# Optimization experiments

Measured on AMD Instinct MI355X. Metric: run time of the kernel, lower is better.

The kernel has to match this reference:

```python
import jax, jax.numpy as jnp
import numpy as np

T, B, I, H = 2048, 64, 512, 512
SIGMA = 0.01


def setup_inputs() -> dict:
    key = jax.random.key(0)
    ks = jax.random.split(key, 9)
    d = {
        "X": jax.random.normal(ks[0], (T, B, I), dtype=jnp.float32),
        "W_xf": jax.random.normal(ks[1], (I, H), dtype=jnp.float32) * SIGMA,
        "W_hf": jax.random.normal(ks[2], (H, H), dtype=jnp.float32) * SIGMA,
        "b_f": jnp.ones((H,), dtype=jnp.float32),
        "W_xi": jax.random.normal(ks[3], (I, H), dtype=jnp.float32) * SIGMA,
        "W_hi": jax.random.normal(ks[4], (H, H), dtype=jnp.float32) * SIGMA,
        "b_i": jnp.zeros((H,), dtype=jnp.float32),
        "W_xo": jax.random.normal(ks[5], (I, H), dtype=jnp.float32) * SIGMA,
        "W_ho": jax.random.normal(ks[6], (H, H), dtype=jnp.float32) * SIGMA,
        "b_o": jnp.zeros((H,), dtype=jnp.float32),
        "W_xc": jax.random.normal(ks[7], (I, H), dtype=jnp.float32) * SIGMA,
        "W_hc": jax.random.normal(ks[8], (H, H), dtype=jnp.float32) * SIGMA,
        "b_c": jnp.zeros((H,), dtype=jnp.float32),
    }
    return d


def reference(X, W_xf, W_hf, b_f, W_xi, W_hi, b_i, W_xo, W_ho, b_o, W_xc, W_hc, b_c):
    batch = X.shape[1]
    hidden = W_hf.shape[0]
    # Fuse the 4 input-side GEMMs into one [T*B, I] @ [I, 4H] GEMM (same math,
    # just batched over time since X is not part of the recurrence).
    W_x = jnp.concatenate([W_xf, W_xi, W_xo, W_xc], axis=1)           # [I, 4H]
    W_h = jnp.concatenate([W_hf, W_hi, W_ho, W_hc], axis=1)           # [H, 4H]
    b = jnp.concatenate([b_f, b_i, b_o, b_c], axis=0)                 # [4H]
    Xg = jnp.einsum('tbi,ih->tbh', X, W_x) + b                        # [T, B, 4H]

    h0 = jnp.zeros((batch, hidden), dtype=X.dtype)
    c0 = jnp.zeros((batch, hidden), dtype=X.dtype)

    def step(carry, xg):
        h, c = carry
        g = xg + h @ W_h                                              # [B, 4H]
        f = jax.nn.sigmoid(g[:, 0 * hidden:1 * hidden])
        i = jax.nn.sigmoid(g[:, 1 * hidden:2 * hidden])
        o = jax.nn.sigmoid(g[:, 2 * hidden:3 * hidden])
        c_hat = jnp.tanh(g[:, 3 * hidden:4 * hidden])
        c_new = f * c + i * c_hat
        h_new = o * jnp.tanh(c_new)
        return (h_new, c_new), h_new

    (h_T, c_T), outputs = jax.lax.scan(step, (h0, c0), Xg)
    return outputs, h_T, c_T
```

## Files before the change

### kernel.cpp

```cpp
#include <hip/hip_runtime.h>
#include <stdint.h>


typedef __attribute__((ext_vector_type(8))) short short8;
typedef __attribute__((ext_vector_type(4))) float f32x4;

#define T_STEPS 2048
#define GB 4
#define GH 64
#define FSTRIDE 16

__device__ __forceinline__ unsigned short f2bf(float f) {
  unsigned int x = __float_as_uint(f);
  x += 0x7fffu + ((x >> 16) & 1u);
  return (unsigned short)(x >> 16);
}
__device__ __forceinline__ float bf2f(unsigned short u) {
  return __uint_as_float(((unsigned int)u) << 16);
}
__device__ __forceinline__ void gl2lds16(const void* g, void* lds) {
  __builtin_amdgcn_global_load_lds(
      (const __attribute__((address_space(1))) void*)(uintptr_t)g,
      (__attribute__((address_space(3))) void*)(unsigned int)(uintptr_t)lds,
      16, 0, 0);
}


__global__ __launch_bounds__(256) void cast_x_kernel(
    const float* __restrict__ X, unsigned short* __restrict__ Xb) {
  long long i = ((long long)blockIdx.x * 256 + threadIdx.x) * 8;
  float4 a = *(const float4*)(X + i);
  float4 b = *(const float4*)(X + i + 4);
  union { short8 v; unsigned short u[8]; } o;
  o.u[0] = f2bf(a.x); o.u[1] = f2bf(a.y); o.u[2] = f2bf(a.z); o.u[3] = f2bf(a.w);
  o.u[4] = f2bf(b.x); o.u[5] = f2bf(b.y); o.u[6] = f2bf(b.z); o.u[7] = f2bf(b.w);
  *(short8*)(Xb + i) = o.v;
}

__global__ __launch_bounds__(256) void pack_w_kernel(
    const float* __restrict__ Wf, const float* __restrict__ Wi,
    const float* __restrict__ Wo, const float* __restrict__ Wc,
    unsigned short* __restrict__ Wt) {
  int n = blockIdx.x;
  int g = n >> 9, h = n & 511;
  const float* W = (g == 0) ? Wf : (g == 1) ? Wi : (g == 2) ? Wo : Wc;
  for (int k = threadIdx.x; k < 512; k += 256)
    Wt[(size_t)n * 512 + k] = f2bf(W[(size_t)k * 512 + h]);
}

__global__ __launch_bounds__(256) void init_kernel(unsigned short* hbuf, int* flags) {
  int i = blockIdx.x * 256 + threadIdx.x;
  if (i < 2 * 64 * 512) hbuf[i] = 0;
  if (i < GB * GH * FSTRIDE) flags[i] = 0;
}

__global__ __launch_bounds__(256) void gemm_xg_kernel(
    const unsigned short* __restrict__ A, const unsigned short* __restrict__ Bt,
    unsigned short* __restrict__ C) {
  __shared__ unsigned short As[128 * 64];
  __shared__ unsigned short Bs[128 * 64];
  const int tid = threadIdx.x;
  const int lane = tid & 63, wave = tid >> 6;
  const int bm = blockIdx.x, bn = blockIdx.y;
  const int wm = (wave & 1) * 64, wn = (wave >> 1) * 64;

  f32x4 acc[4][4];
#pragma unroll
  for (int i = 0; i < 4; ++i)
#pragma unroll
    for (int j = 0; j < 4; ++j) acc[i][j] = (f32x4){0.f, 0.f, 0.f, 0.f};

  for (int kt = 0; kt < 512; kt += 64) {
    __syncthreads();
#pragma unroll
    for (int r = 0; r < 4; ++r) {
      int chunk = r * 256 + tid;
      int row = chunk >> 3, c8 = chunk & 7;
      gl2lds16(A + ((size_t)(bm * 128 + row) * 512 + kt + c8 * 8),
               (void*)(As + (size_t)(r * 256 + wave * 64) * 8));
      gl2lds16(Bt + ((size_t)(bn * 128 + row) * 512 + kt + c8 * 8),
               (void*)(Bs + (size_t)(r * 256 + wave * 64) * 8));
    }
    __syncthreads();
#pragma unroll
    for (int kc = 0; kc < 64; kc += 32) {
      const int ko = kc + (lane >> 4) * 8;
      short8 av[4], bv[4];
#pragma unroll
      for (int mt = 0; mt < 4; ++mt)
        av[mt] = *(const short8*)(As + (wm + mt * 16 + (lane & 15)) * 64 + ko);
#pragma unroll
      for (int nt = 0; nt < 4; ++nt)
        bv[nt] = *(const short8*)(Bs + (wn + nt * 16 + (lane & 15)) * 64 + ko);
#pragma unroll
      for (int mt = 0; mt < 4; ++mt)
#pragma unroll
        for (int nt = 0; nt < 4; ++nt)
          acc[mt][nt] = __builtin_amdgcn_mfma_f32_16x16x32_bf16(
              av[mt], bv[nt], acc[mt][nt], 0, 0, 0);
    }
  }
  const int q = lane >> 4, cidx = lane & 15;
#pragma unroll
  for (int mt = 0; mt < 4; ++mt)
#pragma unroll
    for (int nt = 0; nt < 4; ++nt)
#pragma unroll
      for (int r = 0; r < 4; ++r) {
        int row = wm + mt * 16 + q * 4 + r;
        int col = wn + nt * 16 + cidx;
        C[(size_t)(bm * 128 + row) * 2048 + bn * 128 + col] = f2bf(acc[mt][nt][r]);
      }
}

__global__ __launch_bounds__(256) void lstm_rec_kernel(
    const unsigned short* __restrict__ Xg,
    const unsigned short* __restrict__ Wht,
    const float* __restrict__ b_f, const float* __restrict__ b_i,
    const float* __restrict__ b_o, const float* __restrict__ b_c,
    float* __restrict__ out, unsigned short* hbuf, int* flags) {
  const int tid = threadIdx.x;
  const int lane = tid & 63, wave = tid >> 6;
  const int gb = blockIdx.x >> 6;
  const int gh = blockIdx.x & 63;

  __shared__ unsigned short Wl[32][520];
  __shared__ float Cred[4][16][33];

  for (int idx = tid; idx < 32 * 64; idx += 256) {
    int cc = idx >> 6, k8 = idx & 63;
    int n = (cc >> 3) * 512 + gh * 8 + (cc & 7);
    short8 v = *(const short8*)(Wht + (size_t)n * 512 + k8 * 8);
    *(short8*)(&Wl[cc][k8 * 8]) = v;
  }

  float creg = 0.f;
  float bias0 = 0.f, bias1 = 0.f, bias2 = 0.f, bias3 = 0.f;
  int bb = 0, jj = 0;
  if (tid < 128) {
    bb = tid >> 3; jj = tid & 7;
    int col = gh * 8 + jj;
    bias0 = b_f[col]; bias1 = b_i[col]; bias2 = b_o[col]; bias3 = b_c[col];
  }
  __syncthreads();

  const int myflag = (gb * GH + gh) * FSTRIDE;

  for (int t = 0; t < T_STEPS; ++t) {
    float xg0 = 0.f, xg1 = 0.f, xg2 = 0.f, xg3 = 0.f;
    if (tid < 128) {
      const unsigned short* xr =
          Xg + ((size_t)t * 64 + gb * 16 + bb) * 2048 + gh * 8 + jj;
      xg0 = bf2f(xr[0]); xg1 = bf2f(xr[512]); xg2 = bf2f(xr[1024]); xg3 = bf2f(xr[1536]);
    }
    if (t > 0) {
      if (tid < GH) {
        const int* fp = flags + (gb * GH + tid) * FSTRIDE;
        while (__hip_atomic_load(fp, __ATOMIC_RELAXED, __HIP_MEMORY_SCOPE_AGENT) < t)
          __builtin_amdgcn_s_sleep(1);
      }
      __syncthreads();
      __builtin_amdgcn_fence(__ATOMIC_ACQUIRE, "workgroup");
    }
    const unsigned short* hrow =
        hbuf + ((size_t)(t & 1) * 64 * 512) + (size_t)gb * 16 * 512;
    f32x4 acc0 = {0.f, 0.f, 0.f, 0.f}, acc1 = {0.f, 0.f, 0.f, 0.f};
    const int m = lane & 15, quad = lane >> 4;
#pragma unroll
    for (int kc = 0; kc < 128; kc += 32) {
      int k = wave * 128 + kc + quad * 8;
      const unsigned long long* ap =
          (const unsigned long long*)(hrow + (size_t)m * 512 + k);
      union { short8 v; unsigned long long q[2]; } au;
      au.q[0] = __hip_atomic_load(ap, __ATOMIC_RELAXED, __HIP_MEMORY_SCOPE_AGENT);
      au.q[1] = __hip_atomic_load(ap + 1, __ATOMIC_RELAXED, __HIP_MEMORY_SCOPE_AGENT);
      short8 bfr0 = *(const short8*)(&Wl[m][k]);
      short8 bfr1 = *(const short8*)(&Wl[16 + m][k]);
      acc0 = __builtin_amdgcn_mfma_f32_16x16x32_bf16(au.v, bfr0, acc0, 0, 0, 0);
      acc1 = __builtin_amdgcn_mfma_f32_16x16x32_bf16(au.v, bfr1, acc1, 0, 0, 0);
    }
#pragma unroll
    for (int r = 0; r < 4; ++r) {
      Cred[wave][quad * 4 + r][m] = acc0[r];
      Cred[wave][quad * 4 + r][16 + m] = acc1[r];
    }
    __syncthreads();
    if (tid < 128) {
      float gf = Cred[0][bb][jj] + Cred[1][bb][jj] + Cred[2][bb][jj] + Cred[3][bb][jj];
      float gi = Cred[0][bb][8+jj] + Cred[1][bb][8+jj] + Cred[2][bb][8+jj] + Cred[3][bb][8+jj];
      float go = Cred[0][bb][16+jj] + Cred[1][bb][16+jj] + Cred[2][bb][16+jj] + Cred[3][bb][16+jj];
      float gc = Cred[0][bb][24+jj] + Cred[1][bb][24+jj] + Cred[2][bb][24+jj] + Cred[3][bb][24+jj];
      gf += bias0 + xg0; gi += bias1 + xg1; go += bias2 + xg2; gc += bias3 + xg3;
      float f  = 1.f / (1.f + __expf(-gf));
      float ii = 1.f / (1.f + __expf(-gi));
      float oo = 1.f / (1.f + __expf(-go));
      float ch = 1.f - 2.f / (1.f + __expf(2.f * gc));
      creg = f * creg + ii * ch;
      float tc = 1.f - 2.f / (1.f + __expf(2.f * creg));
      float h = oo * tc;
      size_t orow = ((size_t)t * 64 + gb * 16 + bb) * 512 + gh * 8 + jj;
      out[orow] = h;
      __hip_atomic_store(hbuf + ((size_t)((t + 1) & 1) * 64 * 512) +
                             (size_t)(gb * 16 + bb) * 512 + gh * 8 + jj,
                         f2bf(h), __ATOMIC_RELAXED, __HIP_MEMORY_SCOPE_AGENT);
      if (t == T_STEPS - 1) {
        size_t base = (size_t)T_STEPS * 64 * 512;
        out[base + (size_t)(gb * 16 + bb) * 512 + gh * 8 + jj] = h;
        out[base + 64 * 512 + (size_t)(gb * 16 + bb) * 512 + gh * 8 + jj] = creg;
      }
    }
    __syncthreads();
    __builtin_amdgcn_fence(__ATOMIC_RELEASE, "workgroup");
    if (tid == 0)
      __hip_atomic_store(flags + myflag, t + 1, __ATOMIC_RELAXED,
                         __HIP_MEMORY_SCOPE_AGENT);
  }
}


extern "C" void kernel_launch(void* const* d_in, const int* in_sizes, int n_in,
                              void* d_out, int out_size, void* d_ws, size_t ws_size,
                              hipStream_t stream) {
  const float* X    = (const float*)d_in[0];
  const float* W_xf = (const float*)d_in[1];
  const float* W_hf = (const float*)d_in[2];
  const float* b_f  = (const float*)d_in[3];
  const float* W_xi = (const float*)d_in[4];
  const float* W_hi = (const float*)d_in[5];
  const float* b_i  = (const float*)d_in[6];
  const float* W_xo = (const float*)d_in[7];
  const float* W_ho = (const float*)d_in[8];
  const float* b_o  = (const float*)d_in[9];
  const float* W_xc = (const float*)d_in[10];
  const float* W_hc = (const float*)d_in[11];
  const float* b_c  = (const float*)d_in[12];
  float* out = (float*)d_out;

  char* ws = (char*)d_ws;
  unsigned short* Xb   = (unsigned short*)(ws + 0LL);
  unsigned short* Xg   = (unsigned short*)(ws + 134217728LL);
  unsigned short* Wxt  = (unsigned short*)(ws + 671088640LL);
  unsigned short* Wht  = (unsigned short*)(ws + 673185792LL);
  unsigned short* hbuf = (unsigned short*)(ws + 675282944LL);
  int* flags           = (int*)(ws + 675414016LL);

  cast_x_kernel<<<dim3(32768), dim3(256), 0, stream>>>(X, Xb);
  pack_w_kernel<<<dim3(2048), dim3(256), 0, stream>>>(W_xf, W_xi, W_xo, W_xc, Wxt);
  pack_w_kernel<<<dim3(2048), dim3(256), 0, stream>>>(W_hf, W_hi, W_ho, W_hc, Wht);
  init_kernel<<<dim3(256), dim3(256), 0, stream>>>(hbuf, flags);
  gemm_xg_kernel<<<dim3(1024, 16), dim3(256), 0, stream>>>(Xb, Wxt, Xg);
  lstm_rec_kernel<<<dim3(256), dim3(256), 0, stream>>>(Xg, Wht, b_f, b_i, b_o, b_c,
                                                       out, hbuf, flags);
}
```

Baseline: 5.993 ms.

## Replace per-block flag barrier with step-tagged hidden-state words

Drops the per-block flag array and its spin-wait barrier. Each hidden value is now stored as a 32-bit word holding the bf16 value and the low 16 bits of the step index. Consumers spin directly on the words they read until every tag matches the current step, which removes the flag poll, a block barrier and the release/acquire fences from the critical path. In exchange each h read is twice as wide and split into eight 32-bit atomic loads with a retry loop. hbuf is moved to reuse the start of the workspace (the Xb region) and is initialised after the GEMM.

```diff
diff --git a/kernel.cpp b/kernel.cpp
--- a/kernel.cpp
+++ b/kernel.cpp
@@ -6,9 +6,7 @@
 typedef __attribute__((ext_vector_type(4))) float f32x4;
 
 #define T_STEPS 2048
-#define GB 4
-#define GH 64
-#define FSTRIDE 16
+#define SLOT (64 * 512)
 
 __device__ __forceinline__ unsigned short f2bf(float f) {
   unsigned int x = __float_as_uint(f);
@@ -48,10 +46,9 @@
     Wt[(size_t)n * 512 + k] = f2bf(W[(size_t)k * 512 + h]);
 }
 
-__global__ __launch_bounds__(256) void init_kernel(unsigned short* hbuf, int* flags) {
+__global__ __launch_bounds__(256) void init_kernel(unsigned int* hbuf) {
   int i = blockIdx.x * 256 + threadIdx.x;
-  if (i < 2 * 64 * 512) hbuf[i] = 0;
-  if (i < GB * GH * FSTRIDE) flags[i] = 0;
+  if (i < 2 * SLOT) hbuf[i] = 0u;
 }
 
 __global__ __launch_bounds__(256) void gemm_xg_kernel(
@@ -118,7 +115,7 @@
     const unsigned short* __restrict__ Wht,
     const float* __restrict__ b_f, const float* __restrict__ b_i,
     const float* __restrict__ b_o, const float* __restrict__ b_c,
-    float* __restrict__ out, unsigned short* hbuf, int* flags) {
+    float* __restrict__ out, unsigned int* hbuf) {
   const int tid = threadIdx.x;
   const int lane = tid & 63, wave = tid >> 6;
   const int gb = blockIdx.x >> 6;
@@ -144,7 +141,7 @@
   }
   __syncthreads();
 
-  const int myflag = (gb * GH + gh) * FSTRIDE;
+  const int m = lane & 15, quad = lane >> 4;
 
   for (int t = 0; t < T_STEPS; ++t) {
     float xg0 = 0.f, xg1 = 0.f, xg2 = 0.f, xg3 = 0.f;
@@ -153,27 +150,32 @@
           Xg + ((size_t)t * 64 + gb * 16 + bb) * 2048 + gh * 8 + jj;
       xg0 = bf2f(xr[0]); xg1 = bf2f(xr[512]); xg2 = bf2f(xr[1024]); xg3 = bf2f(xr[1536]);
     }
-    if (t > 0) {
-      if (tid < GH) {
-        const int* fp = flags + (gb * GH + tid) * FSTRIDE;
-        while (__hip_atomic_load(fp, __ATOMIC_RELAXED, __HIP_MEMORY_SCOPE_AGENT) < t)
-          __builtin_amdgcn_s_sleep(1);
-      }
-      __syncthreads();
-      __builtin_amdgcn_fence(__ATOMIC_ACQUIRE, "workgroup");
-    }
-    const unsigned short* hrow =
-        hbuf + ((size_t)(t & 1) * 64 * 512) + (size_t)gb * 16 * 512;
+    const unsigned int tg = (unsigned int)t & 0xffffu;
+    const unsigned int* hcur =
+        hbuf + (size_t)(t & 1) * SLOT + (size_t)(gb * 16 + m) * 512;
     f32x4 acc0 = {0.f, 0.f, 0.f, 0.f}, acc1 = {0.f, 0.f, 0.f, 0.f};
-    const int m = lane & 15, quad = lane >> 4;
 #pragma unroll
     for (int kc = 0; kc < 128; kc += 32) {
-      int k = wave * 128 + kc + quad * 8;
-      const unsigned long long* ap =
-          (const unsigned long long*)(hrow + (size_t)m * 512 + k);
-      union { short8 v; unsigned long long q[2]; } au;
-      au.q[0] = __hip_atomic_load(ap, __ATOMIC_RELAXED, __HIP_MEMORY_SCOPE_AGENT);
-      au.q[1] = __hip_atomic_load(ap + 1, __ATOMIC_RELAXED, __HIP_MEMORY_SCOPE_AGENT);
+      const int k = wave * 128 + kc + quad * 8;
+      const unsigned int* ap = hcur + k;
+      unsigned int w0, w1, w2, w3, w4, w5, w6, w7, bad;
+      do {
+        w0 = __hip_atomic_load(ap + 0, __ATOMIC_RELAXED, __HIP_MEMORY_SCOPE_AGENT);
+        w1 = __hip_atomic_load(ap + 1, __ATOMIC_RELAXED, __HIP_MEMORY_SCOPE_AGENT);
+        w2 = __hip_atomic_load(ap + 2, __ATOMIC_RELAXED, __HIP_MEMORY_SCOPE_AGENT);
+        w3 = __hip_atomic_load(ap + 3, __ATOMIC_RELAXED, __HIP_MEMORY_SCOPE_AGENT);
+        w4 = __hip_atomic_load(ap + 4, __ATOMIC_RELAXED, __HIP_MEMORY_SCOPE_AGENT);
+        w5 = __hip_atomic_load(ap + 5, __ATOMIC_RELAXED, __HIP_MEMORY_SCOPE_AGENT);
+        w6 = __hip_atomic_load(ap + 6, __ATOMIC_RELAXED, __HIP_MEMORY_SCOPE_AGENT);
+        w7 = __hip_atomic_load(ap + 7, __ATOMIC_RELAXED, __HIP_MEMORY_SCOPE_AGENT);
+        bad = ((w0 ^ tg) | (w1 ^ tg) | (w2 ^ tg) | (w3 ^ tg) |
+               (w4 ^ tg) | (w5 ^ tg) | (w6 ^ tg) | (w7 ^ tg)) & 0xffffu;
+      } while (bad != 0u);
+      union { short8 v; unsigned int u[4]; } au;
+      au.u[0] = (w0 >> 16) | (w1 & 0xffff0000u);
+      au.u[1] = (w2 >> 16) | (w3 & 0xffff0000u);
+      au.u[2] = (w4 >> 16) | (w5 & 0xffff0000u);
+      au.u[3] = (w6 >> 16) | (w7 & 0xffff0000u);
       short8 bfr0 = *(const short8*)(&Wl[m][k]);
       short8 bfr1 = *(const short8*)(&Wl[16 + m][k]);
       acc0 = __builtin_amdgcn_mfma_f32_16x16x32_bf16(au.v, bfr0, acc0, 0, 0, 0);
@@ -200,9 +202,11 @@
       float h = oo * tc;
       size_t orow = ((size_t)t * 64 + gb * 16 + bb) * 512 + gh * 8 + jj;
       out[orow] = h;
-      __hip_atomic_store(hbuf + ((size_t)((t + 1) & 1) * 64 * 512) +
+      unsigned int word =
+          ((unsigned int)f2bf(h) << 16) | ((unsigned int)(t + 1) & 0xffffu);
+      __hip_atomic_store(hbuf + (size_t)((t + 1) & 1) * SLOT +
                              (size_t)(gb * 16 + bb) * 512 + gh * 8 + jj,
-                         f2bf(h), __ATOMIC_RELAXED, __HIP_MEMORY_SCOPE_AGENT);
+                         word, __ATOMIC_RELAXED, __HIP_MEMORY_SCOPE_AGENT);
       if (t == T_STEPS - 1) {
         size_t base = (size_t)T_STEPS * 64 * 512;
         out[base + (size_t)(gb * 16 + bb) * 512 + gh * 8 + jj] = h;
@@ -210,10 +214,6 @@
       }
     }
     __syncthreads();
-    __builtin_amdgcn_fence(__ATOMIC_RELEASE, "workgroup");
-    if (tid == 0)
-      __hip_atomic_store(flags + myflag, t + 1, __ATOMIC_RELAXED,
-                         __HIP_MEMORY_SCOPE_AGENT);
   }
 }
 
@@ -241,14 +241,13 @@
   unsigned short* Xg   = (unsigned short*)(ws + 134217728LL);
   unsigned short* Wxt  = (unsigned short*)(ws + 671088640LL);
   unsigned short* Wht  = (unsigned short*)(ws + 673185792LL);
-  unsigned short* hbuf = (unsigned short*)(ws + 675282944LL);
-  int* flags           = (int*)(ws + 675414016LL);
+  unsigned int* hbuf   = (unsigned int*)(ws + 0LL);
 
   cast_x_kernel<<<dim3(32768), dim3(256), 0, stream>>>(X, Xb);
   pack_w_kernel<<<dim3(2048), dim3(256), 0, stream>>>(W_xf, W_xi, W_xo, W_xc, Wxt);
   pack_w_kernel<<<dim3(2048), dim3(256), 0, stream>>>(W_hf, W_hi, W_ho, W_hc, Wht);
-  init_kernel<<<dim3(256), dim3(256), 0, stream>>>(hbuf, flags);
   gemm_xg_kernel<<<dim3(1024, 16), dim3(256), 0, stream>>>(Xb, Wxt, Xg);
+  init_kernel<<<dim3(256), dim3(256), 0, stream>>>(hbuf);
   lstm_rec_kernel<<<dim3(256), dim3(256), 0, stream>>>(Xg, Wht, b_f, b_i, b_o, b_c,
-                                                       out, hbuf, flags);
-}
+                                                       out, hbuf);
+}
```

New measurement: 12.66 ms. 2.11x slower.

## Repartition LSTM recurrence to 64 blocks with register-resident recurrent weights

Applied to the files above, without the earlier changes.

The recurrent kernel moves from 256 blocks (8 hidden columns each) to 64 blocks (32 hidden columns each). Each wave owns one gate and holds its slice of W_h in registers, which removes the LDS weight reads and the cross-wave K reduction. Fewer blocks means fewer flags to poll per step, and the spin loop no longer sleeps. The h loads now use cache-bypassing inline asm, and hbuf and flags are placed in the workspace region of Xb, which is dead once the GEMM has run. The cost is heavy register pressure and more MFMA work per block on the serial step path.

```diff
diff --git a/kernel.cpp b/kernel.cpp
--- a/kernel.cpp
+++ b/kernel.cpp
@@ -4,11 +4,9 @@
 
 typedef __attribute__((ext_vector_type(8))) short short8;
 typedef __attribute__((ext_vector_type(4))) float f32x4;
+typedef __attribute__((ext_vector_type(4))) unsigned int u32x4;
 
 #define T_STEPS 2048
-#define GB 4
-#define GH 64
-#define FSTRIDE 16
 
 __device__ __forceinline__ unsigned short f2bf(float f) {
   unsigned int x = __float_as_uint(f);
@@ -48,10 +46,10 @@
     Wt[(size_t)n * 512 + k] = f2bf(W[(size_t)k * 512 + h]);
 }
 
-__global__ __launch_bounds__(256) void init_kernel(unsigned short* hbuf, int* flags) {
+__global__ __launch_bounds__(256) void init_kernel(unsigned int* hbuf, int* flags) {
   int i = blockIdx.x * 256 + threadIdx.x;
-  if (i < 2 * 64 * 512) hbuf[i] = 0;
-  if (i < GB * GH * FSTRIDE) flags[i] = 0;
+  if (i < 2 * 64 * 256) hbuf[i] = 0u;
+  if (i < 64) flags[i] = 0;
 }
 
 __global__ __launch_bounds__(256) void gemm_xg_kernel(
@@ -113,107 +111,119 @@
       }
 }
 
-__global__ __launch_bounds__(256) void lstm_rec_kernel(
+__global__ __launch_bounds__(256, 1) void lstm_rec_kernel(
     const unsigned short* __restrict__ Xg,
     const unsigned short* __restrict__ Wht,
     const float* __restrict__ b_f, const float* __restrict__ b_i,
     const float* __restrict__ b_o, const float* __restrict__ b_c,
-    float* __restrict__ out, unsigned short* hbuf, int* flags) {
+    float* __restrict__ out, unsigned int* hbuf, int* flags) {
   const int tid = threadIdx.x;
   const int lane = tid & 63, wave = tid >> 6;
-  const int gb = blockIdx.x >> 6;
-  const int gh = blockIdx.x & 63;
-
-  __shared__ unsigned short Wl[32][520];
-  __shared__ float Cred[4][16][33];
-
-  for (int idx = tid; idx < 32 * 64; idx += 256) {
-    int cc = idx >> 6, k8 = idx & 63;
-    int n = (cc >> 3) * 512 + gh * 8 + (cc & 7);
-    short8 v = *(const short8*)(Wht + (size_t)n * 512 + k8 * 8);
-    *(short8*)(&Wl[cc][k8 * 8]) = v;
+  const int gb = blockIdx.x >> 4;
+  const int gh = blockIdx.x & 15;
+  const int m = lane & 15, quad = lane >> 4;
+
+  __shared__ float Glds[4][16][34];
+
+  short8 bw0[16], bw1[16];
+  {
+    const unsigned short* wb = Wht + ((size_t)wave * 512 + gh * 32) * 512;
+#pragma unroll
+    for (int s = 0; s < 16; ++s) {
+      bw0[s] = *(const short8*)(wb + (size_t)m * 512 + s * 32 + quad * 8);
+      bw1[s] = *(const short8*)(wb + (size_t)(16 + m) * 512 + s * 32 + quad * 8);
+    }
   }
 
-  float creg = 0.f;
-  float bias0 = 0.f, bias1 = 0.f, bias2 = 0.f, bias3 = 0.f;
-  int bb = 0, jj = 0;
-  if (tid < 128) {
-    bb = tid >> 3; jj = tid & 7;
-    int col = gh * 8 + jj;
-    bias0 = b_f[col]; bias1 = b_i[col]; bias2 = b_o[col]; bias3 = b_c[col];
-  }
-  __syncthreads();
-
-  const int myflag = (gb * GH + gh) * FSTRIDE;
+  const int b = tid >> 4, p = tid & 15;
+  const int j0 = gh * 32 + 2 * p;
+  const float2 bf_f = *(const float2*)(b_f + j0);
+  const float2 bf_i = *(const float2*)(b_i + j0);
+  const float2 bf_o = *(const float2*)(b_o + j0);
+  const float2 bf_c = *(const float2*)(b_c + j0);
+  float c0 = 0.f, c1 = 0.f;
+
+  const int myflag = gb * 16 + gh;
 
   for (int t = 0; t < T_STEPS; ++t) {
-    float xg0 = 0.f, xg1 = 0.f, xg2 = 0.f, xg3 = 0.f;
-    if (tid < 128) {
-      const unsigned short* xr =
-          Xg + ((size_t)t * 64 + gb * 16 + bb) * 2048 + gh * 8 + jj;
-      xg0 = bf2f(xr[0]); xg1 = bf2f(xr[512]); xg2 = bf2f(xr[1024]); xg3 = bf2f(xr[1536]);
+    unsigned int xgw0, xgw1, xgw2, xgw3;
+    {
+      const unsigned int* xr =
+          (const unsigned int*)(Xg + ((size_t)t * 64 + gb * 16 + b) * 2048) +
+          gh * 16 + p;
+      xgw0 = xr[0]; xgw1 = xr[256]; xgw2 = xr[512]; xgw3 = xr[768];
     }
     if (t > 0) {
-      if (tid < GH) {
-        const int* fp = flags + (gb * GH + tid) * FSTRIDE;
-        while (__hip_atomic_load(fp, __ATOMIC_RELAXED, __HIP_MEMORY_SCOPE_AGENT) < t)
-          __builtin_amdgcn_s_sleep(1);
+      if (tid < 16) {
+        const int* fp = flags + gb * 16 + tid;
+        while (__hip_atomic_load(fp, __ATOMIC_RELAXED,
+                                 __HIP_MEMORY_SCOPE_AGENT) < t) {}
       }
       __syncthreads();
       __builtin_amdgcn_fence(__ATOMIC_ACQUIRE, "workgroup");
     }
-    const unsigned short* hrow =
-        hbuf + ((size_t)(t & 1) * 64 * 512) + (size_t)gb * 16 * 512;
+    const char* hq = (const char*)hbuf + (size_t)(t & 1) * 65536 +
+                     (size_t)(gb * 16 + m) * 1024 + (size_t)quad * 16;
+    u32x4 hv[16];
+#pragma unroll
+    for (int s = 0; s < 16; ++s)
+      asm volatile("global_load_dwordx4 %0, %1, off sc0 sc1"
+                   : "=&v"(hv[s]) : "v"(hq + s * 64) : "memory");
+    asm volatile("s_waitcnt vmcnt(0)" ::: "memory");
+    __builtin_amdgcn_sched_barrier(0);
+
     f32x4 acc0 = {0.f, 0.f, 0.f, 0.f}, acc1 = {0.f, 0.f, 0.f, 0.f};
-    const int m = lane & 15, quad = lane >> 4;
-#pragma unroll
-    for (int kc = 0; kc < 128; kc += 32) {
-      int k = wave * 128 + kc + quad * 8;
-      const unsigned long long* ap =
-          (const unsigned long long*)(hrow + (size_t)m * 512 + k);
-      union { short8 v; unsigned long long q[2]; } au;
-      au.q[0] = __hip_atomic_load(ap, __ATOMIC_RELAXED, __HIP_MEMORY_SCOPE_AGENT);
-      au.q[1] = __hip_atomic_load(ap + 1, __ATOMIC_RELAXED, __HIP_MEMORY_SCOPE_AGENT);
-      short8 bfr0 = *(const short8*)(&Wl[m][k]);
-      short8 bfr1 = *(const short8*)(&Wl[16 + m][k]);
-      acc0 = __builtin_amdgcn_mfma_f32_16x16x32_bf16(au.v, bfr0, acc0, 0, 0, 0);
-      acc1 = __builtin_amdgcn_mfma_f32_16x16x32_bf16(au.v, bfr1, acc1, 0, 0, 0);
+#pragma unroll
+    for (int s = 0; s < 16; ++s) {
+      union { u32x4 u; short8 v; } au;
+      au.u = hv[s];
+      acc0 = __builtin_amdgcn_mfma_f32_16x16x32_bf16(au.v, bw0[s], acc0, 0, 0, 0);
+      acc1 = __builtin_amdgcn_mfma_f32_16x16x32_bf16(au.v, bw1[s], acc1, 0, 0, 0);
     }
 #pragma unroll
     for (int r = 0; r < 4; ++r) {
-      Cred[wave][quad * 4 + r][m] = acc0[r];
-      Cred[wave][quad * 4 + r][16 + m] = acc1[r];
-    }
-    __syncthreads();
-    if (tid < 128) {
-      float gf = Cred[0][bb][jj] + Cred[1][bb][jj] + Cred[2][bb][jj] + Cred[3][bb][jj];
-      float gi = Cred[0][bb][8+jj] + Cred[1][bb][8+jj] + Cred[2][bb][8+jj] + Cred[3][bb][8+jj];
-      float go = Cred[0][bb][16+jj] + Cred[1][bb][16+jj] + Cred[2][bb][16+jj] + Cred[3][bb][16+jj];
-      float gc = Cred[0][bb][24+jj] + Cred[1][bb][24+jj] + Cred[2][bb][24+jj] + Cred[3][bb][24+jj];
-      gf += bias0 + xg0; gi += bias1 + xg1; go += bias2 + xg2; gc += bias3 + xg3;
-      float f  = 1.f / (1.f + __expf(-gf));
-      float ii = 1.f / (1.f + __expf(-gi));
-      float oo = 1.f / (1.f + __expf(-go));
-      float ch = 1.f - 2.f / (1.f + __expf(2.f * gc));
-      creg = f * creg + ii * ch;
-      float tc = 1.f - 2.f / (1.f + __expf(2.f * creg));
-      float h = oo * tc;
-      size_t orow = ((size_t)t * 64 + gb * 16 + bb) * 512 + gh * 8 + jj;
-      out[orow] = h;
-      __hip_atomic_store(hbuf + ((size_t)((t + 1) & 1) * 64 * 512) +
-                             (size_t)(gb * 16 + bb) * 512 + gh * 8 + jj,
-                         f2bf(h), __ATOMIC_RELAXED, __HIP_MEMORY_SCOPE_AGENT);
-      if (t == T_STEPS - 1) {
-        size_t base = (size_t)T_STEPS * 64 * 512;
-        out[base + (size_t)(gb * 16 + bb) * 512 + gh * 8 + jj] = h;
-        out[base + 64 * 512 + (size_t)(gb * 16 + bb) * 512 + gh * 8 + jj] = creg;
-      }
-    }
+      Glds[wave][quad * 4 + r][m] = acc0[r];
+      Glds[wave][quad * 4 + r][16 + m] = acc1[r];
+    }
+    __syncthreads();
+    float2 vf = *(const float2*)&Glds[0][b][2 * p];
+    float2 vi = *(const float2*)&Glds[1][b][2 * p];
+    float2 vo = *(const float2*)&Glds[2][b][2 * p];
+    float2 vc = *(const float2*)&Glds[3][b][2 * p];
+    float gf0 = vf.x + bf_f.x + bf2f((unsigned short)(xgw0 & 0xffff));
+    float gf1 = vf.y + bf_f.y + bf2f((unsigned short)(xgw0 >> 16));
+    float gi0 = vi.x + bf_i.x + bf2f((unsigned short)(xgw1 & 0xffff));
+    float gi1 = vi.y + bf_i.y + bf2f((unsigned short)(xgw1 >> 16));
+    float go0 = vo.x + bf_o.x + bf2f((unsigned short)(xgw2 & 0xffff));
+    float go1 = vo.y + bf_o.y + bf2f((unsigned short)(xgw2 >> 16));
+    float gc0 = vc.x + bf_c.x + bf2f((unsigned short)(xgw3 & 0xffff));
+    float gc1 = vc.y + bf_c.y + bf2f((unsigned short)(xgw3 >> 16));
+    float f0 = 1.f / (1.f + __expf(-gf0)), f1 = 1.f / (1.f + __expf(-gf1));
+    float i0 = 1.f / (1.f + __expf(-gi0)), i1 = 1.f / (1.f + __expf(-gi1));
+    float o0 = 1.f / (1.f + __expf(-go0)), o1 = 1.f / (1.f + __expf(-go1));
+    float ch0 = 1.f - 2.f / (1.f + __expf(2.f * gc0));
+    float ch1 = 1.f - 2.f / (1.f + __expf(2.f * gc1));
+    c0 = f0 * c0 + i0 * ch0;
+    c1 = f1 * c1 + i1 * ch1;
+    float h0 = o0 * (1.f - 2.f / (1.f + __expf(2.f * c0)));
+    float h1 = o1 * (1.f - 2.f / (1.f + __expf(2.f * c1)));
+    unsigned int hword = ((unsigned int)f2bf(h1) << 16) | (unsigned int)f2bf(h0);
+    __hip_atomic_store(hbuf + (size_t)((t + 1) & 1) * 16384 +
+                           (size_t)(gb * 16 + b) * 256 + gh * 16 + p,
+                       hword, __ATOMIC_RELAXED, __HIP_MEMORY_SCOPE_AGENT);
     __syncthreads();
     __builtin_amdgcn_fence(__ATOMIC_RELEASE, "workgroup");
     if (tid == 0)
       __hip_atomic_store(flags + myflag, t + 1, __ATOMIC_RELAXED,
                          __HIP_MEMORY_SCOPE_AGENT);
+    float2 h2; h2.x = h0; h2.y = h1;
+    *(float2*)(out + ((size_t)t * 64 + gb * 16 + b) * 512 + j0) = h2;
+    if (t == T_STEPS - 1) {
+      size_t base = (size_t)T_STEPS * 64 * 512;
+      *(float2*)(out + base + (size_t)(gb * 16 + b) * 512 + j0) = h2;
+      float2 c2; c2.x = c0; c2.y = c1;
+      *(float2*)(out + base + 64 * 512 + (size_t)(gb * 16 + b) * 512 + j0) = c2;
+    }
   }
 }
 
@@ -241,14 +251,14 @@
   unsigned short* Xg   = (unsigned short*)(ws + 134217728LL);
   unsigned short* Wxt  = (unsigned short*)(ws + 671088640LL);
   unsigned short* Wht  = (unsigned short*)(ws + 673185792LL);
-  unsigned short* hbuf = (unsigned short*)(ws + 675282944LL);
-  int* flags           = (int*)(ws + 675414016LL);
+  unsigned int* hbuf   = (unsigned int*)(ws + 0LL);
+  int* flags           = (int*)(ws + 131072LL);
 
   cast_x_kernel<<<dim3(32768), dim3(256), 0, stream>>>(X, Xb);
   pack_w_kernel<<<dim3(2048), dim3(256), 0, stream>>>(W_xf, W_xi, W_xo, W_xc, Wxt);
   pack_w_kernel<<<dim3(2048), dim3(256), 0, stream>>>(W_hf, W_hi, W_ho, W_hc, Wht);
-  init_kernel<<<dim3(256), dim3(256), 0, stream>>>(hbuf, flags);
   gemm_xg_kernel<<<dim3(1024, 16), dim3(256), 0, stream>>>(Xb, Wxt, Xg);
-  lstm_rec_kernel<<<dim3(256), dim3(256), 0, stream>>>(Xg, Wht, b_f, b_i, b_o, b_c,
-                                                       out, hbuf, flags);
-}
+  init_kernel<<<dim3(128), dim3(256), 0, stream>>>(hbuf, flags);
+  lstm_rec_kernel<<<dim3(64), dim3(256), 0, stream>>>(Xg, Wht, b_f, b_i, b_o, b_c,
+                                                      out, hbuf, flags);
+}
```

Measured after the change: 8.609 ms. 1.44x slower.
